# Kernel tuning notes

Hardware: AMD Instinct MI355X
Metric: run time of the kernel (lower is better)

## Reference

```python
import jax, jax.numpy as jnp
import numpy as np

DIM = 1024
NUM_HEADS = 16
HEAD_DIM = DIM // NUM_HEADS
B, N = 4, 2048


def _rope_sin_cos(seq_len, head_dim, dtype=jnp.float32):
    inv_freq = 1.0 / (10000.0 ** (jnp.arange(0, head_dim, 2, dtype=jnp.float32) / head_dim))
    t = jnp.arange(seq_len, dtype=jnp.float32)
    freqs = jnp.einsum('i,j->ij', t, inv_freq)          # [N, head_dim/2]
    emb = jnp.concatenate([freqs, freqs], axis=-1)      # [N, head_dim]
    return jnp.sin(emb).astype(dtype), jnp.cos(emb).astype(dtype)


def _rotate_half(x):
    x1, x2 = jnp.split(x, 2, axis=-1)
    return jnp.concatenate([-x2, x1], axis=-1)


def setup_inputs() -> dict:
    key = jax.random.key(0)
    k1, k2, k3, k4, k5 = jax.random.split(key, 5)
    scale = 0.02
    return {
        'x': jax.random.normal(k1, (B, N, DIM), dtype=jnp.float32),
        'W_qkv': jax.random.normal(k2, (DIM, 3 * DIM), dtype=jnp.float32) * scale,
        'b_qkv': jax.random.normal(k3, (3 * DIM,), dtype=jnp.float32) * scale,
        'W_proj': jax.random.normal(k4, (DIM, DIM), dtype=jnp.float32) * scale,
        'b_proj': jax.random.normal(k5, (DIM,), dtype=jnp.float32) * scale,
    }


def reference(x, W_qkv, b_qkv, W_proj, b_proj):
    Bsz, Nlen, C = x.shape
    H, Dh = NUM_HEADS, HEAD_DIM
    qkv = x @ W_qkv + b_qkv                              # [B, N, 3C]
    q, k, v = jnp.split(qkv, 3, axis=-1)
    # [B, H, N, Dh]
    q = q.reshape(Bsz, Nlen, H, Dh).transpose(0, 2, 1, 3)
    k = k.reshape(Bsz, Nlen, H, Dh).transpose(0, 2, 1, 3)
    v = v.reshape(Bsz, Nlen, H, Dh).transpose(0, 2, 1, 3)
    sin, cos = _rope_sin_cos(Nlen, Dh, x.dtype)          # [N, Dh] each, broadcast
    q = q * cos + _rotate_half(q) * sin
    k = k * cos + _rotate_half(k) * sin
    scale = 1.0 / jnp.sqrt(jnp.asarray(Dh, x.dtype))
    scores = jnp.einsum('bhqd,bhkd->bhqk', q, k) * scale  # [B, H, N, N]
    attn = jax.nn.softmax(scores, axis=-1)
    out = jnp.einsum('bhqk,bhkd->bhqd', attn, v)          # [B, H, N, Dh]
    out = out.transpose(0, 2, 1, 3).reshape(Bsz, Nlen, C)
    return out @ W_proj + b_proj
```

## Files before the change

kernel.cpp:

```cpp
#include <hip/hip_runtime.h>
#include <hip/hip_bf16.h>
#include <math.h>

#define BSZ 4
#define NSEQ 2048
#define CDIM 1024
#define NH 16
#define DH 64
#define KC 64
#define KMAX_STRIDE 32

typedef _Float16 half8_t __attribute__((ext_vector_type(8)));
typedef _Float16 half4_t __attribute__((ext_vector_type(4)));
typedef __fp16 pk2_t __attribute__((ext_vector_type(2)));
typedef __fp16 pk4_t __attribute__((ext_vector_type(4)));
typedef float floatx4 __attribute__((ext_vector_type(4)));

#define GLOBAL_AS(p) ((const __attribute__((address_space(1))) void*)(p))
#define LDS_AS(p)    ((__attribute__((address_space(3))) void*)(p))

__global__ __launch_bounds__(256) void prep_kernel(
    const float* __restrict__ x, const float* __restrict__ Wqkv,
    const float* __restrict__ Wproj, _Float16* __restrict__ xh,
    _Float16* __restrict__ Wt, _Float16* __restrict__ Wpt,
    float2* __restrict__ ropet, unsigned* __restrict__ kmaxu) {
  __shared__ float Ls[64][65];
  const int t = threadIdx.x;
  const int bid = blockIdx.x;

  if (bid < 4096) {
    const size_t i = ((size_t)bid * 256 + t) * 8;
    float4 a = *(const float4*)(x + i);
    float4 b = *(const float4*)(x + i + 4);
    half8_t h;
    h[0] = (_Float16)a.x; h[1] = (_Float16)a.y; h[2] = (_Float16)a.z; h[3] = (_Float16)a.w;
    h[4] = (_Float16)b.x; h[5] = (_Float16)b.y; h[6] = (_Float16)b.z; h[7] = (_Float16)b.w;
    *(half8_t*)(xh + i) = h;
    return;
  }
  if (bid >= 5120) {
    const int idx = (bid - 5120) * 256 + t;
    const int n = idx >> 5, f = idx & 31;
    const float invf = expf(-9.210340371976184f * ((float)f * (1.0f / 32.0f)));
    float s, c;
    sincosf((float)n * invf, &s, &c);
    ropet[idx] = make_float2(c, s);
    if (bid == 5120)
      for (int i2 = t; i2 < 64 * KMAX_STRIDE; i2 += 256) kmaxu[i2] = 0u;
    return;
  }
  const float* src;
  _Float16* dst;
  int R, C, bx, by;
  if (bid < 4864) {
    src = Wqkv; dst = Wt; R = 1024; C = 3072;
    bx = (bid - 4096) % 48; by = (bid - 4096) / 48;
  } else {
    src = Wproj; dst = Wpt; R = 1024; C = 1024;
    bx = (bid - 4864) % 16; by = (bid - 4864) / 16;
  }
  const int r0 = by * 64, c0 = bx * 64;
  {
    const int lr = t >> 2, lcg = (t & 3) * 16;
    const float* s = src + (size_t)(r0 + lr) * C + c0 + lcg;
#pragma unroll
    for (int u = 0; u < 4; ++u)
      *(float4*)&Ls[lr][lcg + 4 * u] = *(const float4*)(s + 4 * u);
  }
  __syncthreads();
  const int c = t >> 2, rg = (t & 3) * 16;
  half8_t h0, h1;
#pragma unroll
  for (int u = 0; u < 8; ++u) h0[u] = (_Float16)Ls[rg + u][c];
#pragma unroll
  for (int u = 0; u < 8; ++u) h1[u] = (_Float16)Ls[rg + 8 + u][c];
  _Float16* d = dst + (size_t)(c0 + c) * R + r0 + rg;
  *(half8_t*)d = h0;
  *(half8_t*)(d + 8) = h1;
}

__global__ __launch_bounds__(256) void qkv_gemm_kernel(
    const _Float16* __restrict__ xh, const _Float16* __restrict__ Wt,
    const float* __restrict__ bias, const float2* __restrict__ rope,
    _Float16* __restrict__ Qh, _Float16* __restrict__ Kh,
    _Float16* __restrict__ Vh, float* __restrict__ qn,
    unsigned* __restrict__ kmaxu) {
  __shared__ _Float16 smem[16384];
  _Float16* As = smem;
  _Float16* Bs = smem + 8192;
  const int tid = threadIdx.x;
  const int lane = tid & 63, w = tid >> 6;
  const int m = lane & 15, quad = lane >> 4;
  const int wr = (w >> 1) * 64, wc = (w & 1) * 64;
  const int m0 = blockIdx.y * 128;
  const int N0 = blockIdx.x * 128;
  const int sr = lane >> 3, sc = (lane & 7) * 8;

  floatx4 acc[4][4];
#pragma unroll
  for (int i = 0; i < 4; ++i)
#pragma unroll
    for (int j = 0; j < 4; ++j) acc[i][j] = (floatx4){0.f, 0.f, 0.f, 0.f};

  for (int k0 = 0; k0 < CDIM; k0 += 64) {
    __syncthreads();
#pragma unroll
    for (int i = 0; i < 4; ++i) {
      const int row = (w * 4 + i) * 8 + sr;
      __builtin_amdgcn_global_load_lds(
          GLOBAL_AS(xh + (size_t)(m0 + row) * CDIM + k0 + sc),
          LDS_AS(As + (w * 4 + i) * 512), 16, 0, 0);
      __builtin_amdgcn_global_load_lds(
          GLOBAL_AS(Wt + (size_t)(N0 + row) * CDIM + k0 + sc),
          LDS_AS(Bs + (w * 4 + i) * 512), 16, 0, 0);
    }
    __syncthreads();
#pragma unroll
    for (int ks = 0; ks < 2; ++ks) {
      half8_t af[4], bf[4];
#pragma unroll
      for (int mt = 0; mt < 4; ++mt)
        af[mt] = *(half8_t*)(As + (wr + mt * 16 + m) * 64 + ks * 32 + quad * 8);
#pragma unroll
      for (int nt = 0; nt < 4; ++nt)
        bf[nt] = *(half8_t*)(Bs + (wc + nt * 16 + m) * 64 + ks * 32 + quad * 8);
#pragma unroll
      for (int mt = 0; mt < 4; ++mt)
#pragma unroll
        for (int nt = 0; nt < 4; ++nt)
          acc[mt][nt] = __builtin_amdgcn_mfma_f32_16x16x32_f16(
              af[mt], bf[nt], acc[mt][nt], 0, 0, 0);
    }
  }

  const int F0 = N0 + wc;
  const int which = F0 >> 10;
  const int head = (F0 & 1023) >> 6;
  float bv[4];
#pragma unroll
  for (int nt = 0; nt < 4; ++nt) bv[nt] = bias[F0 + nt * 16 + m];

  if (which == 2) {
    _Float16* Vl = smem;
    const int bb = m0 >> 11, n0 = m0 & 2047;
    const int head_base = (N0 & 1023) >> 6;
#pragma unroll
    for (int hl = 0; hl < 2; ++hl) {
      __syncthreads();
      if ((w & 1) == hl) {
#pragma unroll
        for (int mt = 0; mt < 4; ++mt)
#pragma unroll
          for (int nt = 0; nt < 4; ++nt) {
            half4_t h4;
#pragma unroll
            for (int reg = 0; reg < 4; ++reg)
              h4[reg] = (_Float16)(acc[mt][nt][reg] + bv[nt]);
            *(half4_t*)(Vl + (nt * 16 + m) * 132 + wr + mt * 16 + 4 * quad) = h4;
          }
      }
      __syncthreads();
      const size_t vrow = (size_t)(bb * NH + head_base + hl) * DH;
#pragma unroll
      for (int p = 0; p < 4; ++p) {
        const int idx = p * 256 + tid;
        const int d = idx >> 4, ch = idx & 15;
        half8_t v = *(half8_t*)(Vl + d * 132 + ch * 8);
        *(half8_t*)(Vh + (vrow + d) * NSEQ + n0 + ch * 8) = v;
      }
    }
  } else {
    _Float16* dst = which ? Kh : Qh;
    const float qs = which ? 1.0f : 0.125f * 1.4426950408889634f;
    float ssum[4][4];
#pragma unroll
    for (int mt = 0; mt < 4; ++mt)
#pragma unroll
      for (int reg = 0; reg < 4; ++reg) ssum[mt][reg] = 0.f;
#pragma unroll
    for (int mt = 0; mt < 4; ++mt)
#pragma unroll
      for (int reg = 0; reg < 4; ++reg) {
        const int gm = m0 + wr + mt * 16 + 4 * quad + reg;
        const int b = gm >> 11, n = gm & 2047;
        const float2 csA = rope[n * 32 + m];
        const float2 csB = rope[n * 32 + 16 + m];
        const size_t obase = ((size_t)(b * NH + head) * NSEQ + n) * DH;
#pragma unroll
        for (int nt = 0; nt < 4; ++nt) {
          const float val = acc[mt][nt][reg] + bv[nt];
          const float rot = (nt < 2) ? -(acc[mt][nt + 2][reg] + bv[nt + 2])
                                     :  (acc[mt][nt - 2][reg] + bv[nt - 2]);
          const float sv = (nt & 1) ? csB.y : csA.y;
          const float cv = (nt & 1) ? csB.x : csA.x;
          const _Float16 h16 = (_Float16)((val * cv + rot * sv) * qs);
          dst[obase + nt * 16 + m] = h16;
          const float vv = (float)h16;
          ssum[mt][reg] += vv * vv;
        }
      }
#pragma unroll
    for (int mt = 0; mt < 4; ++mt)
#pragma unroll
      for (int reg = 0; reg < 4; ++reg) {
        float s = ssum[mt][reg];
        s += __shfl_xor(s, 1, 64);
        s += __shfl_xor(s, 2, 64);
        s += __shfl_xor(s, 4, 64);
        s += __shfl_xor(s, 8, 64);
        ssum[mt][reg] = s;
      }
    if (which == 0) {
      if (m == 0) {
#pragma unroll
        for (int mt = 0; mt < 4; ++mt)
#pragma unroll
          for (int reg = 0; reg < 4; ++reg) {
            const int gm = m0 + wr + mt * 16 + 4 * quad + reg;
            const int b = gm >> 11, n = gm & 2047;
            qn[(size_t)(b * NH + head) * NSEQ + n] = sqrtf(ssum[mt][reg]);
          }
      }
    } else {
      float mx = 0.f;
#pragma unroll
      for (int mt = 0; mt < 4; ++mt)
#pragma unroll
        for (int reg = 0; reg < 4; ++reg) mx = fmaxf(mx, ssum[mt][reg]);
      mx = fmaxf(mx, __shfl_xor(mx, 16, 64));
      mx = fmaxf(mx, __shfl_xor(mx, 32, 64));
      if (lane == 0) {
        const int b = m0 >> 11;
        atomicMax(&kmaxu[(b * NH + head) * KMAX_STRIDE],
                  __float_as_uint(sqrtf(mx)));
      }
    }
  }
}

__global__ __launch_bounds__(512, 8) void attn_kernel(
    const _Float16* __restrict__ Qh, const _Float16* __restrict__ Kh,
    const _Float16* __restrict__ Vh, const float* __restrict__ qn,
    const unsigned* __restrict__ kmaxu, _Float16* __restrict__ AO) {
  __shared__ _Float16 smem[17408];
  float* Os = (float*)smem;
  _Float16* Ks = smem;
  _Float16* Vt = smem + 4608;

  const int tid = threadIdx.x;
  const int lane = tid & 63;
  const int w = tid >> 6;
  const int m = lane & 15;
  const int quad = lane >> 4;

  const int bid = blockIdx.x;
  const int slot = bid & 7, kk = bid >> 3;
  const int bh = slot + 8 * (kk >> 4);
  const int q0 = (kk & 15) * 128;

  const _Float16* Qb = Qh + (size_t)bh * NSEQ * DH;
  const _Float16* Kb = Kh + (size_t)bh * NSEQ * DH;
  const _Float16* Vb = Vh + (size_t)bh * DH * NSEQ;

  const int rA = q0 + w * 16 + m;
  half8_t qfA0 = *(const half8_t*)(Qb + (size_t)rA * DH + quad * 8);
  half8_t qfA1 = *(const half8_t*)(Qb + (size_t)rA * DH + 32 + quad * 8);

  const float kmx = __uint_as_float(kmaxu[bh * KMAX_STRIDE]);
  const float mA = qn[(size_t)bh * NSEQ + rA] * kmx;

  const int skey = tid >> 3, sdg = (tid & 7) * 8;
  const _Float16* ksrc = Kb + (size_t)skey * DH + sdg;
  const _Float16* vsrc = Vb + (size_t)skey * NSEQ + sdg;
  const int koff = skey * 72 + sdg;

  float lA = 0.f;
  floatx4 OA[4];
#pragma unroll
  for (int nb = 0; nb < 4; ++nb) OA[nb] = (floatx4){0.f, 0.f, 0.f, 0.f};
  const pk2_t one2 = {(__fp16)1.f, (__fp16)1.f};

  const int NCK = NSEQ / KC;
  for (int ck = 0; ck < NCK; ++ck) {
    half8_t k8 = *(const half8_t*)ksrc;  ksrc += KC * DH;
    half8_t v8 = *(const half8_t*)vsrc;  vsrc += KC;
    __syncthreads();
    *(half8_t*)(Ks + koff) = k8;
    *(half8_t*)(Vt + koff) = v8;
    __syncthreads();

#pragma unroll
    for (int kt = 0; kt < 4; ++kt) {
      half8_t kf0 = *(half8_t*)(Ks + (kt * 16 + m) * 72 + quad * 8);
      half8_t kf1 = *(half8_t*)(Ks + (kt * 16 + m) * 72 + 32 + quad * 8);
      __builtin_amdgcn_s_setprio(1);
      floatx4 a = (floatx4){-mA, -mA, -mA, -mA};
      a = __builtin_amdgcn_mfma_f32_16x16x32_f16(kf0, qfA0, a, 0, 0, 0);
      a = __builtin_amdgcn_mfma_f32_16x16x32_f16(kf1, qfA1, a, 0, 0, 0);
      __builtin_amdgcn_s_setprio(0);

      pk2_t a01 = __builtin_amdgcn_cvt_pkrtz(__builtin_exp2f(a[0]),
                                             __builtin_exp2f(a[1]));
      pk2_t a23 = __builtin_amdgcn_cvt_pkrtz(__builtin_exp2f(a[2]),
                                             __builtin_exp2f(a[3]));
      lA = __builtin_amdgcn_fdot2(a01, one2, lA, false);
      lA = __builtin_amdgcn_fdot2(a23, one2, lA, false);
      half4_t phA = __builtin_bit_cast(
          half4_t, (pk4_t)__builtin_shufflevector(a01, a23, 0, 1, 2, 3));

      __builtin_amdgcn_s_setprio(1);
#pragma unroll
      for (int nb = 0; nb < 4; ++nb) {
        half4_t vf = *(half4_t*)(Vt + (nb * 16 + m) * 72 + kt * 16 + quad * 4);
        OA[nb] = __builtin_amdgcn_mfma_f32_16x16x16f16(phA, vf, OA[nb], 0, 0, 0);
      }
      __builtin_amdgcn_s_setprio(0);
    }
  }

  lA += __shfl_xor(lA, 16, 64); lA += __shfl_xor(lA, 32, 64);
  float lA4[4];
#pragma unroll
  for (int r = 0; r < 4; ++r) lA4[r] = __shfl(lA, 4 * quad + r, 64);

  const int b = bh >> 4, h = bh & 15;
  const int ql = tid >> 2, dgo = (tid & 3) * 16;
  const int gq = q0 + ql;
  _Float16* dst = AO + ((size_t)(b * NSEQ + gq)) * CDIM + h * DH + dgo;

  __syncthreads();
#pragma unroll
  for (int nb = 0; nb < 4; ++nb)
#pragma unroll
    for (int r = 0; r < 4; ++r)
      Os[(w * 16 + 4 * quad + r) * 68 + nb * 16 + m] = OA[nb][r] * (1.0f / lA4[r]);
  __syncthreads();
#pragma unroll
  for (int u = 0; u < 2; ++u) {
    half8_t o;
#pragma unroll
    for (int v = 0; v < 8; ++v) o[v] = (_Float16)Os[ql * 68 + dgo + u * 8 + v];
    *(half8_t*)(dst + u * 8) = o;
  }
}

__global__ __launch_bounds__(256) void proj_gemm_kernel(
    const _Float16* __restrict__ Ah, const _Float16* __restrict__ Wt,
    const float* __restrict__ bias, float* __restrict__ out) {
  __shared__ _Float16 As[128 * 64];
  __shared__ _Float16 Bs[128 * 64];
  const int tid = threadIdx.x;
  const int lane = tid & 63, w = tid >> 6;
  const int m = lane & 15, quad = lane >> 4;
  const int wr = (w >> 1) * 64, wc = (w & 1) * 64;
  const int m0 = blockIdx.y * 128;
  const int N0 = blockIdx.x * 128;
  const int sr = lane >> 3, sc = (lane & 7) * 8;

  floatx4 acc[4][4];
#pragma unroll
  for (int i = 0; i < 4; ++i)
#pragma unroll
    for (int j = 0; j < 4; ++j) acc[i][j] = (floatx4){0.f, 0.f, 0.f, 0.f};

  for (int k0 = 0; k0 < CDIM; k0 += 64) {
    __syncthreads();
#pragma unroll
    for (int i = 0; i < 4; ++i) {
      const int row = (w * 4 + i) * 8 + sr;
      __builtin_amdgcn_global_load_lds(
          GLOBAL_AS(Ah + (size_t)(m0 + row) * CDIM + k0 + sc),
          LDS_AS(As + (w * 4 + i) * 512), 16, 0, 0);
      __builtin_amdgcn_global_load_lds(
          GLOBAL_AS(Wt + (size_t)(N0 + row) * CDIM + k0 + sc),
          LDS_AS(Bs + (w * 4 + i) * 512), 16, 0, 0);
    }
    __syncthreads();
#pragma unroll
    for (int ks = 0; ks < 2; ++ks) {
      half8_t af[4], bf[4];
#pragma unroll
      for (int mt = 0; mt < 4; ++mt)
        af[mt] = *(half8_t*)(As + (wr + mt * 16 + m) * 64 + ks * 32 + quad * 8);
#pragma unroll
      for (int nt = 0; nt < 4; ++nt)
        bf[nt] = *(half8_t*)(Bs + (wc + nt * 16 + m) * 64 + ks * 32 + quad * 8);
#pragma unroll
      for (int mt = 0; mt < 4; ++mt)
#pragma unroll
        for (int nt = 0; nt < 4; ++nt)
          acc[mt][nt] = __builtin_amdgcn_mfma_f32_16x16x32_f16(
              af[mt], bf[nt], acc[mt][nt], 0, 0, 0);
    }
  }

  const int F0 = N0 + wc;
  float bv[4];
#pragma unroll
  for (int nt = 0; nt < 4; ++nt) bv[nt] = bias[F0 + nt * 16 + m];
#pragma unroll
  for (int mt = 0; mt < 4; ++mt)
#pragma unroll
    for (int reg = 0; reg < 4; ++reg) {
      const int gm = m0 + wr + mt * 16 + 4 * quad + reg;
#pragma unroll
      for (int nt = 0; nt < 4; ++nt)
        out[(size_t)gm * CDIM + F0 + nt * 16 + m] = acc[mt][nt][reg] + bv[nt];
    }
}

extern "C" void kernel_launch(void* const* d_in, const int* in_sizes, int n_in,
                              void* d_out, int out_size, void* d_ws, size_t ws_size,
                              hipStream_t stream) {
  const float* x     = (const float*)d_in[0];
  const float* Wqkv  = (const float*)d_in[1];
  const float* bqkv  = (const float*)d_in[2];
  const float* Wproj = (const float*)d_in[3];
  const float* bproj = (const float*)d_in[4];
  float* out = (float*)d_out;

  const size_t per = (size_t)BSZ * NH * NSEQ * DH;
  _Float16* xh  = (_Float16*)d_ws;
  _Float16* Wt  = xh + per;
  _Float16* Wpt = Wt + (size_t)3072 * 1024;
  _Float16* Qh  = Wpt + (size_t)1024 * 1024;
  _Float16* Kh  = Qh + per;
  _Float16* Vh  = Kh + per;
  _Float16* AOh = Vh + per;
  float*    qnp = (float*)(AOh + per);
  unsigned* kmx = (unsigned*)(qnp + (size_t)64 * NSEQ);
  float2*   ropet = (float2*)(kmx + 64 * KMAX_STRIDE);

  prep_kernel<<<5376, 256, 0, stream>>>(x, Wqkv, Wproj, xh, Wt, Wpt, ropet, kmx);
  qkv_gemm_kernel<<<dim3(24, 64), 256, 0, stream>>>(xh, Wt, bqkv, ropet,
                                                    Qh, Kh, Vh, qnp, kmx);
  attn_kernel<<<1024, 512, 0, stream>>>(Qh, Kh, Vh, qnp, kmx, AOh);
  proj_gemm_kernel<<<dim3(8, 64), 256, 0, stream>>>(AOh, Wpt, bproj, out);
}
```

Baseline: 310.6 us.

## Double-buffer GEMM LDS tiles with interleaved prefetch and 256-row blocks

Both the QKV and projection GEMMs switch to 512-thread blocks computing 256x128 tiles. The LDS staging is double-buffered, and the next k-tile's global-to-LDS loads are issued between the fragment reads and the MFMA groups of the current tile. MFMA sections are wrapped in s_setprio, and the V-transpose epilogue is resized for the taller tile. The aim is to hide global load latency and halve the per-iteration barriers, at the cost of more LDS per block (96KB) and fewer blocks in the grid.

```diff
diff --git a/kernel.cpp b/kernel.cpp
--- a/kernel.cpp
+++ b/kernel.cpp
@@ -79,22 +79,20 @@
   *(half8_t*)(d + 8) = h1;
 }
 
-__global__ __launch_bounds__(256) void qkv_gemm_kernel(
+__global__ __launch_bounds__(512, 2) void qkv_gemm_kernel(
     const _Float16* __restrict__ xh, const _Float16* __restrict__ Wt,
     const float* __restrict__ bias, const float2* __restrict__ rope,
     _Float16* __restrict__ Qh, _Float16* __restrict__ Kh,
     _Float16* __restrict__ Vh, float* __restrict__ qn,
     unsigned* __restrict__ kmaxu) {
-  __shared__ _Float16 smem[16384];
-  _Float16* As = smem;
-  _Float16* Bs = smem + 8192;
+  __shared__ _Float16 smem[49152];
   const int tid = threadIdx.x;
   const int lane = tid & 63, w = tid >> 6;
   const int m = lane & 15, quad = lane >> 4;
-  const int wr = (w >> 1) * 64, wc = (w & 1) * 64;
-  const int m0 = blockIdx.y * 128;
+  const int wr = ((w >> 1) & 3) * 64;
+  const int wc = (w & 1) * 64;
+  const int m0 = blockIdx.y * 256;
   const int N0 = blockIdx.x * 128;
-  const int sr = lane >> 3, sc = (lane & 7) * 8;
 
   floatx4 acc[4][4];
 #pragma unroll
@@ -102,36 +100,60 @@
 #pragma unroll
     for (int j = 0; j < 4; ++j) acc[i][j] = (floatx4){0.f, 0.f, 0.f, 0.f};
 
-  for (int k0 = 0; k0 < CDIM; k0 += 64) {
+  auto STAGE1 = [&](int l, int tt, int p) {
+    const int slot0 = l * 512 + w * 64;
+    const int slot = slot0 + lane;
+    const int k0 = tt * 64;
+    if (l < 4) {
+      const int row = slot >> 3, col = (slot & 7) * 8;
+      __builtin_amdgcn_global_load_lds(
+          GLOBAL_AS(xh + (size_t)(m0 + row) * CDIM + k0 + col),
+          LDS_AS(smem + p * 16384 + slot0 * 8), 16, 0, 0);
+    } else {
+      const int bs = slot - 2048;
+      const int row = bs >> 3, col = (bs & 7) * 8;
+      __builtin_amdgcn_global_load_lds(
+          GLOBAL_AS(Wt + (size_t)(N0 + row) * CDIM + k0 + col),
+          LDS_AS(smem + 32768 + p * 8192 + (slot0 - 2048) * 8), 16, 0, 0);
+    }
+  };
+
+#pragma unroll
+  for (int l = 0; l < 6; ++l) STAGE1(l, 0, 0);
+
+  for (int t = 0; t < 16; ++t) {
+    const int cur = t & 1;
     __syncthreads();
 #pragma unroll
-    for (int i = 0; i < 4; ++i) {
-      const int row = (w * 4 + i) * 8 + sr;
-      __builtin_amdgcn_global_load_lds(
-          GLOBAL_AS(xh + (size_t)(m0 + row) * CDIM + k0 + sc),
-          LDS_AS(As + (w * 4 + i) * 512), 16, 0, 0);
-      __builtin_amdgcn_global_load_lds(
-          GLOBAL_AS(Wt + (size_t)(N0 + row) * CDIM + k0 + sc),
-          LDS_AS(Bs + (w * 4 + i) * 512), 16, 0, 0);
-    }
-    __syncthreads();
-#pragma unroll
-    for (int ks = 0; ks < 2; ++ks) {
-      half8_t af[4], bf[4];
-#pragma unroll
-      for (int mt = 0; mt < 4; ++mt)
-        af[mt] = *(half8_t*)(As + (wr + mt * 16 + m) * 64 + ks * 32 + quad * 8);
-#pragma unroll
-      for (int nt = 0; nt < 4; ++nt)
-        bf[nt] = *(half8_t*)(Bs + (wc + nt * 16 + m) * 64 + ks * 32 + quad * 8);
-#pragma unroll
-      for (int mt = 0; mt < 4; ++mt)
-#pragma unroll
-        for (int nt = 0; nt < 4; ++nt)
-          acc[mt][nt] = __builtin_amdgcn_mfma_f32_16x16x32_f16(
-              af[mt], bf[nt], acc[mt][nt], 0, 0, 0);
-    }
-  }
+    for (int q = 0; q < 4; ++q) {
+      const int qm = q >> 1, qn = q & 1;
+      half8_t af[2][2], bf[2][2];
+#pragma unroll
+      for (int i = 0; i < 2; ++i)
+#pragma unroll
+        for (int ks = 0; ks < 2; ++ks) {
+          af[i][ks] = *(half8_t*)(smem + cur * 16384 +
+                                  (wr + (qm * 2 + i) * 16 + m) * 64 + ks * 32 + quad * 8);
+          bf[i][ks] = *(half8_t*)(smem + 32768 + cur * 8192 +
+                                  (wc + (qn * 2 + i) * 16 + m) * 64 + ks * 32 + quad * 8);
+        }
+      if (t + 1 < 16 && q < 3) {
+        STAGE1(2 * q, t + 1, cur ^ 1);
+        STAGE1(2 * q + 1, t + 1, cur ^ 1);
+      }
+      __builtin_amdgcn_s_setprio(1);
+#pragma unroll
+      for (int i = 0; i < 2; ++i)
+#pragma unroll
+        for (int j = 0; j < 2; ++j)
+#pragma unroll
+          for (int ks = 0; ks < 2; ++ks)
+            acc[qm * 2 + i][qn * 2 + j] = __builtin_amdgcn_mfma_f32_16x16x32_f16(
+                af[i][ks], bf[j][ks], acc[qm * 2 + i][qn * 2 + j], 0, 0, 0);
+      __builtin_amdgcn_s_setprio(0);
+    }
+  }
+  __syncthreads();
 
   const int F0 = N0 + wc;
   const int which = F0 >> 10;
@@ -146,7 +168,7 @@
     const int head_base = (N0 & 1023) >> 6;
 #pragma unroll
     for (int hl = 0; hl < 2; ++hl) {
-      __syncthreads();
+      if (hl) __syncthreads();
       if ((w & 1) == hl) {
 #pragma unroll
         for (int mt = 0; mt < 4; ++mt)
@@ -156,16 +178,16 @@
 #pragma unroll
             for (int reg = 0; reg < 4; ++reg)
               h4[reg] = (_Float16)(acc[mt][nt][reg] + bv[nt]);
-            *(half4_t*)(Vl + (nt * 16 + m) * 132 + wr + mt * 16 + 4 * quad) = h4;
+            *(half4_t*)(Vl + (nt * 16 + m) * 260 + wr + mt * 16 + 4 * quad) = h4;
           }
       }
       __syncthreads();
       const size_t vrow = (size_t)(bb * NH + head_base + hl) * DH;
 #pragma unroll
       for (int p = 0; p < 4; ++p) {
-        const int idx = p * 256 + tid;
-        const int d = idx >> 4, ch = idx & 15;
-        half8_t v = *(half8_t*)(Vl + d * 132 + ch * 8);
+        const int idx = p * 512 + tid;
+        const int d = idx >> 5, ch = idx & 31;
+        half8_t v = *(half8_t*)(Vl + d * 260 + ch * 8);
         *(half8_t*)(Vh + (vrow + d) * NSEQ + n0 + ch * 8) = v;
       }
     }
@@ -344,18 +366,17 @@
   }
 }
 
-__global__ __launch_bounds__(256) void proj_gemm_kernel(
+__global__ __launch_bounds__(512, 2) void proj_gemm_kernel(
     const _Float16* __restrict__ Ah, const _Float16* __restrict__ Wt,
     const float* __restrict__ bias, float* __restrict__ out) {
-  __shared__ _Float16 As[128 * 64];
-  __shared__ _Float16 Bs[128 * 64];
+  __shared__ _Float16 smem[49152];
   const int tid = threadIdx.x;
   const int lane = tid & 63, w = tid >> 6;
   const int m = lane & 15, quad = lane >> 4;
-  const int wr = (w >> 1) * 64, wc = (w & 1) * 64;
-  const int m0 = blockIdx.y * 128;
+  const int wr = ((w >> 1) & 3) * 64;
+  const int wc = (w & 1) * 64;
+  const int m0 = blockIdx.y * 256;
   const int N0 = blockIdx.x * 128;
-  const int sr = lane >> 3, sc = (lane & 7) * 8;
 
   floatx4 acc[4][4];
 #pragma unroll
@@ -363,34 +384,57 @@
 #pragma unroll
     for (int j = 0; j < 4; ++j) acc[i][j] = (floatx4){0.f, 0.f, 0.f, 0.f};
 
-  for (int k0 = 0; k0 < CDIM; k0 += 64) {
+  auto STAGE1 = [&](int l, int tt, int p) {
+    const int slot0 = l * 512 + w * 64;
+    const int slot = slot0 + lane;
+    const int k0 = tt * 64;
+    if (l < 4) {
+      const int row = slot >> 3, col = (slot & 7) * 8;
+      __builtin_amdgcn_global_load_lds(
+          GLOBAL_AS(Ah + (size_t)(m0 + row) * CDIM + k0 + col),
+          LDS_AS(smem + p * 16384 + slot0 * 8), 16, 0, 0);
+    } else {
+      const int bs = slot - 2048;
+      const int row = bs >> 3, col = (bs & 7) * 8;
+      __builtin_amdgcn_global_load_lds(
+          GLOBAL_AS(Wt + (size_t)(N0 + row) * CDIM + k0 + col),
+          LDS_AS(smem + 32768 + p * 8192 + (slot0 - 2048) * 8), 16, 0, 0);
+    }
+  };
+
+#pragma unroll
+  for (int l = 0; l < 6; ++l) STAGE1(l, 0, 0);
+
+  for (int t = 0; t < 16; ++t) {
+    const int cur = t & 1;
     __syncthreads();
 #pragma unroll
-    for (int i = 0; i < 4; ++i) {
-      const int row = (w * 4 + i) * 8 + sr;
-      __builtin_amdgcn_global_load_lds(
-          GLOBAL_AS(Ah + (size_t)(m0 + row) * CDIM + k0 + sc),
-          LDS_AS(As + (w * 4 + i) * 512), 16, 0, 0);
-      __builtin_amdgcn_global_load_lds(
-          GLOBAL_AS(Wt + (size_t)(N0 + row) * CDIM + k0 + sc),
-          LDS_AS(Bs + (w * 4 + i) * 512), 16, 0, 0);
-    }
-    __syncthreads();
-#pragma unroll
-    for (int ks = 0; ks < 2; ++ks) {
-      half8_t af[4], bf[4];
-#pragma unroll
-      for (int mt = 0; mt < 4; ++mt)
-        af[mt] = *(half8_t*)(As + (wr + mt * 16 + m) * 64 + ks * 32 + quad * 8);
-#pragma unroll
-      for (int nt = 0; nt < 4; ++nt)
-        bf[nt] = *(half8_t*)(Bs + (wc + nt * 16 + m) * 64 + ks * 32 + quad * 8);
-#pragma unroll
-      for (int mt = 0; mt < 4; ++mt)
-#pragma unroll
-        for (int nt = 0; nt < 4; ++nt)
-          acc[mt][nt] = __builtin_amdgcn_mfma_f32_16x16x32_f16(
-              af[mt], bf[nt], acc[mt][nt], 0, 0, 0);
+    for (int q = 0; q < 4; ++q) {
+      const int qm = q >> 1, qn = q & 1;
+      half8_t af[2][2], bf[2][2];
+#pragma unroll
+      for (int i = 0; i < 2; ++i)
+#pragma unroll
+        for (int ks = 0; ks < 2; ++ks) {
+          af[i][ks] = *(half8_t*)(smem + cur * 16384 +
+                                  (wr + (qm * 2 + i) * 16 + m) * 64 + ks * 32 + quad * 8);
+          bf[i][ks] = *(half8_t*)(smem + 32768 + cur * 8192 +
+                                  (wc + (qn * 2 + i) * 16 + m) * 64 + ks * 32 + quad * 8);
+        }
+      if (t + 1 < 16 && q < 3) {
+        STAGE1(2 * q, t + 1, cur ^ 1);
+        STAGE1(2 * q + 1, t + 1, cur ^ 1);
+      }
+      __builtin_amdgcn_s_setprio(1);
+#pragma unroll
+      for (int i = 0; i < 2; ++i)
+#pragma unroll
+        for (int j = 0; j < 2; ++j)
+#pragma unroll
+          for (int ks = 0; ks < 2; ++ks)
+            acc[qm * 2 + i][qn * 2 + j] = __builtin_amdgcn_mfma_f32_16x16x32_f16(
+                af[i][ks], bf[j][ks], acc[qm * 2 + i][qn * 2 + j], 0, 0, 0);
+      __builtin_amdgcn_s_setprio(0);
     }
   }
 
@@ -432,8 +476,8 @@
   float2*   ropet = (float2*)(kmx + 64 * KMAX_STRIDE);
 
   prep_kernel<<<5376, 256, 0, stream>>>(x, Wqkv, Wproj, xh, Wt, Wpt, ropet, kmx);
-  qkv_gemm_kernel<<<dim3(24, 64), 256, 0, stream>>>(xh, Wt, bqkv, ropet,
+  qkv_gemm_kernel<<<dim3(24, 32), 512, 0, stream>>>(xh, Wt, bqkv, ropet,
                                                     Qh, Kh, Vh, qnp, kmx);
   attn_kernel<<<1024, 512, 0, stream>>>(Qh, Kh, Vh, qnp, kmx, AOh);
-  proj_gemm_kernel<<<dim3(8, 64), 256, 0, stream>>>(AOh, Wpt, bproj, out);
+  proj_gemm_kernel<<<dim3(8, 32), 512, 0, stream>>>(AOh, Wpt, bproj, out);
 }
```

Measured after the change: 346.2 us. 1.11x slower.
